# Performance work log

Hardware: AMD Instinct MI355X
Metric: run time of the kernel (lower is better)

## Reference

```python
import jax, jax.numpy as jnp
import numpy as np

N_NODES = 65536   # sli * node = 512 * 128
N_EDGES = 524288  # avg degree 8
SLI, NODE = 512, 128
SLOPE = 0.01      # nn.LeakyReLU default negative_slope


def leaky_relu(v):
    return jnp.where(v >= 0, v, SLOPE * v)


def graph_conv(h, src, dst, W, b):
    """DGL GraphConv with norm='both': D_in^{-1/2} A D_out^{-1/2} h W + b, then LeakyReLU."""
    ones = jnp.ones(src.shape[0], dtype=h.dtype)
    out_deg = jnp.clip(jax.ops.segment_sum(ones, src, num_segments=N_NODES), 1.0)
    in_deg = jnp.clip(jax.ops.segment_sum(ones, dst, num_segments=N_NODES), 1.0)
    h = h * jax.lax.rsqrt(out_deg)[:, None]                     # src-side norm
    agg = jax.ops.segment_sum(h[src], dst, num_segments=N_NODES)  # gather + scatter-add
    agg = agg * jax.lax.rsqrt(in_deg)[:, None]                  # dst-side norm
    return leaky_relu(agg @ W + b)


def graphsage(x, src, dst, W, b):
    # x: [sli, C, node] -> [sli*node, C] -> GraphConv -> [sli, F, node]
    sli, C, node = x.shape
    h = x.transpose(0, 2, 1).reshape(-1, C)
    h = graph_conv(h, src, dst, W, b)
    return h.reshape(sli, node, -1).transpose(0, 2, 1)


def conv1x1(x, W, b):
    # pointwise Conv1d: x [S, Cin, N], W [Cout, Cin] -> [S, Cout, N]
    return jnp.einsum('scn,oc->son', x, W) + b[None, :, None]


def setup_inputs() -> dict:
    key = jax.random.key(0)
    ks = jax.random.split(key, 16)
    d = {
        'x': jax.random.normal(ks[0], (SLI, 128, NODE), dtype=jnp.float32),
        'edge_src': jax.random.randint(ks[1], (N_EDGES,), 0, N_NODES, dtype=jnp.int32),
        'edge_dst': jax.random.randint(ks[2], (N_EDGES,), 0, N_NODES, dtype=jnp.int32),
        'W_head': jax.random.normal(ks[3], (128, 128), dtype=jnp.float32) * 0.05,
        'b_head': jnp.zeros((128,), dtype=jnp.float32),
        'W_res0': jax.random.normal(ks[4], (128, 128), dtype=jnp.float32) * 0.05,
        'b_res0': jnp.zeros((128,), dtype=jnp.float32),
        'W_res1': jax.random.normal(ks[5], (128, 128), dtype=jnp.float32) * 0.05,
        'b_res1': jnp.zeros((128,), dtype=jnp.float32),
        'W_res2': jax.random.normal(ks[6], (128, 128), dtype=jnp.float32) * 0.05,
        'b_res2': jnp.zeros((128,), dtype=jnp.float32),
        'W_fusion': jax.random.normal(ks[7], (256, 512), dtype=jnp.float32) * 0.05,
        'b_fusion': jnp.zeros((256,), dtype=jnp.float32),
        'W_p1': jax.random.normal(ks[8], (256, 768), dtype=jnp.float32) * 0.05,
        'b_p1': jnp.zeros((256,), dtype=jnp.float32),
        'W_p2': jax.random.normal(ks[9], (64, 256), dtype=jnp.float32) * 0.05,
        'b_p2': jnp.zeros((64,), dtype=jnp.float32),
        'W_p3': jax.random.normal(ks[10], (2, 64), dtype=jnp.float32) * 0.05,
        'b_p3': jnp.zeros((2,), dtype=jnp.float32),
    }
    return d


def reference(x, edge_src, edge_dst, W_head, b_head, W_res0, b_res0, W_res1, b_res1,
              W_res2, b_res2, W_fusion, b_fusion, W_p1, b_p1, W_p2, b_p2, W_p3, b_p3):
    h = graphsage(x, edge_src, edge_dst, W_head, b_head)   # [S, 128, N]
    states = [h]
    for W, b in ((W_res0, b_res0), (W_res1, b_res1), (W_res2, b_res2)):
        h = graphsage(h, edge_src, edge_dst, W, b) + h     # residual
        states.append(h)
    state = jnp.concatenate(states, axis=1)                # [S, 512, N]
    fused = conv1x1(state, W_fusion, b_fusion)             # [S, 256, N]
    global_state = jnp.max(fused, axis=2, keepdims=True)   # [S, 256, 1]
    global_state = jnp.broadcast_to(global_state, (state.shape[0], 256, state.shape[2]))
    state = jnp.concatenate([global_state, state], axis=1) # [S, 768, N]
    y = leaky_relu(conv1x1(state, W_p1, b_p1))
    y = leaky_relu(conv1x1(y, W_p2, b_p2))
    return conv1x1(y, W_p3, b_p3)                          # [S, 2, N]
```

## Files before the change

### kernel.cpp

```cpp
#include <hip/hip_runtime.h>

#define NN 65536
#define NE 524288
#define SLOPE 0.01f

typedef unsigned short us;
typedef __attribute__((ext_vector_type(8))) short short8;
typedef __attribute__((ext_vector_type(4))) float f32x4;

__device__ __forceinline__ float leaky(float v) { return v >= 0.f ? v : SLOPE * v; }
__device__ __forceinline__ float b2f(us u) { return __uint_as_float(((unsigned)u) << 16); }
__device__ __forceinline__ us f2b(float f) {
  unsigned u = __float_as_uint(f);
  u += 0x7fffu + ((u >> 16) & 1u);
  return (us)(u >> 16);
}
__device__ __forceinline__ void split2(float v, us& hi, us& lo) {
  hi = f2b(v);
  lo = f2b(v - b2f(hi));
}

__device__ __forceinline__ void gload16(const void* g, void* l) {
  __builtin_amdgcn_global_load_lds(
      (const __attribute__((address_space(1))) unsigned int*)g,
      (__attribute__((address_space(3))) unsigned int*)l, 16, 0, 0);
}

__global__ void zero_ints(int* __restrict__ p, int n) {
  int i = blockIdx.x * blockDim.x + threadIdx.x;
  if (i < n) p[i] = 0;
}

__global__ void deg_count(const int* __restrict__ src, const int* __restrict__ dst,
                          int* __restrict__ cout, int* __restrict__ cin) {
  int e = blockIdx.x * blockDim.x + threadIdx.x;
  if (e < NE) {
    atomicAdd(&cout[src[e]], 1);
    atomicAdd(&cin[dst[e]], 1);
  }
}

__global__ void rs_kernel(const int* __restrict__ cout, const int* __restrict__ cin,
                          float* __restrict__ rs_out, float* __restrict__ rs_in) {
  int n = blockIdx.x * blockDim.x + threadIdx.x;
  if (n < NN) {
    rs_out[n] = rsqrtf((float)(cout[n] > 0 ? cout[n] : 1));
    rs_in[n]  = rsqrtf((float)(cin[n]  > 0 ? cin[n]  : 1));
  }
}

__global__ __launch_bounds__(1024) void scan_kernel(const int* __restrict__ cnt,
                                                    int* __restrict__ row_ptr) {
  __shared__ int part[1024];
  int t = threadIdx.x;
  int base = t * 64;
  int s = 0;
  for (int i = 0; i < 64; ++i) s += cnt[base + i];
  part[t] = s;
  __syncthreads();
  for (int d = 1; d < 1024; d <<= 1) {
    int v = (t >= d) ? part[t - d] : 0;
    __syncthreads();
    part[t] += v;
    __syncthreads();
  }
  int run = part[t] - s;
  for (int i = 0; i < 64; ++i) { row_ptr[base + i] = run; run += cnt[base + i]; }
  if (t == 1023) row_ptr[NN] = run;
}

__global__ void csr_fill(const int* __restrict__ src, const int* __restrict__ dst,
                         const int* __restrict__ row_ptr, int* __restrict__ cursor,
                         int* __restrict__ csr) {
  int e = blockIdx.x * blockDim.x + threadIdx.x;
  if (e < NE) {
    int d = dst[e];
    int pos = atomicAdd(&cursor[d], 1);
    csr[row_ptr[d] + pos] = src[e];
  }
}

__global__ __launch_bounds__(256) void transpose_x(const float* __restrict__ x,
                                                   us* __restrict__ h0h,
                                                   us* __restrict__ h0l) {
  __shared__ float tile[128][68];
  int s  = blockIdx.x >> 1;
  int vh = (blockIdx.x & 1) * 64;
  const float* xs = x + (size_t)s * 16384;
  int t = threadIdx.x;
  int v4 = t & 15, c0 = t >> 4;
  for (int p = 0; p < 8; ++p) {
    int c = c0 + p * 16;
    float4 val = *(const float4*)(xs + (size_t)c * 128 + vh + v4 * 4);
    *(float4*)&tile[c][v4 * 4] = val;
  }
  __syncthreads();
  int c4 = t & 31, v0 = t >> 5;
  for (int p = 0; p < 8; ++p) {
    int v = v0 + p * 8;
    float o[4];
    o[0] = tile[c4 * 4 + 0][v];
    o[1] = tile[c4 * 4 + 1][v];
    o[2] = tile[c4 * 4 + 2][v];
    o[3] = tile[c4 * 4 + 3][v];
    us hh[4], ll[4];
#pragma unroll
    for (int j = 0; j < 4; ++j) split2(o[j], hh[j], ll[j]);
    size_t off = (size_t)(s * 128 + vh + v) * 128 + c4 * 4;
    uint2 wh = make_uint2((unsigned)hh[0] | ((unsigned)hh[1] << 16),
                          (unsigned)hh[2] | ((unsigned)hh[3] << 16));
    uint2 wl = make_uint2((unsigned)ll[0] | ((unsigned)ll[1] << 16),
                          (unsigned)ll[2] | ((unsigned)ll[3] << 16));
    *(uint2*)(h0h + off) = wh;
    *(uint2*)(h0l + off) = wl;
  }
}

__global__ void wsplit(const float* __restrict__ src, us* __restrict__ bh,
                       us* __restrict__ bl, int N, int K, int ld, int koff) {
  int idx = blockIdx.x * 256 + threadIdx.x;
  if (idx >= N * K) return;
  int n = idx / K, k = idx - n * K;
  float v = src[(size_t)n * ld + koff + k];
  us hi, lo; split2(v, hi, lo);
  bh[idx] = hi; bl[idx] = lo;
}

__global__ void wsplit_t(const float* __restrict__ src, us* __restrict__ bh,
                         us* __restrict__ bl, int N, int K, int ld) {
  int idx = blockIdx.x * 256 + threadIdx.x;
  if (idx >= N * K) return;
  int n = idx / K, k = idx - n * K;
  float v = src[(size_t)k * ld + n];
  us hi, lo; split2(v, hi, lo);
  bh[idx] = hi; bl[idx] = lo;
}

__global__ __launch_bounds__(256) void aggregate(
    const us* __restrict__ hh, const us* __restrict__ hl, int lda,
    const int* __restrict__ row_ptr, const int* __restrict__ csr,
    const float* __restrict__ rs_out, const float* __restrict__ rs_in,
    us* __restrict__ aggh, us* __restrict__ aggl) {
  const int lane = threadIdx.x & 63;
  const int n = blockIdx.x * 4 + (threadIdx.x >> 6);
  const us* base = ((lane < 32) ? hh : hl) + (size_t)(lane & 31) * 4;
  const int b = row_ptr[n], e = row_ptr[n + 1];
  float a0 = 0.f, a1 = 0.f, a2 = 0.f, a3 = 0.f;
  int i = b;
  for (; i + 4 <= e; i += 4) {
    int s0 = csr[i], s1 = csr[i + 1], s2 = csr[i + 2], s3 = csr[i + 3];
    uint2 v0 = *(const uint2*)(base + (size_t)s0 * lda);
    uint2 v1 = *(const uint2*)(base + (size_t)s1 * lda);
    uint2 v2 = *(const uint2*)(base + (size_t)s2 * lda);
    uint2 v3 = *(const uint2*)(base + (size_t)s3 * lda);
    float w0 = rs_out[s0], w1 = rs_out[s1], w2 = rs_out[s2], w3 = rs_out[s3];
    a0 = fmaf(w0, __uint_as_float(v0.x << 16), a0);
    a1 = fmaf(w0, __uint_as_float(v0.x & 0xffff0000u), a1);
    a2 = fmaf(w0, __uint_as_float(v0.y << 16), a2);
    a3 = fmaf(w0, __uint_as_float(v0.y & 0xffff0000u), a3);
    a0 = fmaf(w1, __uint_as_float(v1.x << 16), a0);
    a1 = fmaf(w1, __uint_as_float(v1.x & 0xffff0000u), a1);
    a2 = fmaf(w1, __uint_as_float(v1.y << 16), a2);
    a3 = fmaf(w1, __uint_as_float(v1.y & 0xffff0000u), a3);
    a0 = fmaf(w2, __uint_as_float(v2.x << 16), a0);
    a1 = fmaf(w2, __uint_as_float(v2.x & 0xffff0000u), a1);
    a2 = fmaf(w2, __uint_as_float(v2.y << 16), a2);
    a3 = fmaf(w2, __uint_as_float(v2.y & 0xffff0000u), a3);
    a0 = fmaf(w3, __uint_as_float(v3.x << 16), a0);
    a1 = fmaf(w3, __uint_as_float(v3.x & 0xffff0000u), a1);
    a2 = fmaf(w3, __uint_as_float(v3.y << 16), a2);
    a3 = fmaf(w3, __uint_as_float(v3.y & 0xffff0000u), a3);
  }
  for (; i < e; ++i) {
    int s0 = csr[i];
    uint2 v0 = *(const uint2*)(base + (size_t)s0 * lda);
    float w0 = rs_out[s0];
    a0 = fmaf(w0, __uint_as_float(v0.x << 16), a0);
    a1 = fmaf(w0, __uint_as_float(v0.x & 0xffff0000u), a1);
    a2 = fmaf(w0, __uint_as_float(v0.y << 16), a2);
    a3 = fmaf(w0, __uint_as_float(v0.y & 0xffff0000u), a3);
  }
  a0 += __shfl_xor(a0, 32);
  a1 += __shfl_xor(a1, 32);
  a2 += __shfl_xor(a2, 32);
  a3 += __shfl_xor(a3, 32);
  const float ri = rs_in[n];
  a0 *= ri; a1 *= ri; a2 *= ri; a3 *= ri;
  us h[4], l[4];
  split2(a0, h[0], l[0]); split2(a1, h[1], l[1]);
  split2(a2, h[2], l[2]); split2(a3, h[3], l[3]);
  size_t o = (size_t)n * 128 + (size_t)(lane & 31) * 4;
  if (lane < 32) {
    uint2 wv = make_uint2((unsigned)h[0] | ((unsigned)h[1] << 16),
                          (unsigned)h[2] | ((unsigned)h[3] << 16));
    *(uint2*)(aggh + o) = wv;
  } else {
    uint2 wv = make_uint2((unsigned)l[0] | ((unsigned)l[1] << 16),
                          (unsigned)l[2] | ((unsigned)l[3] << 16));
    *(uint2*)(aggl + o) = wv;
  }
}

template<int KTOT, int BN, int WM, int PH, int MODE>
__global__ __launch_bounds__(512) void mgemm8(
    const us* __restrict__ Ah, const us* __restrict__ Al, int lda,
    const us* __restrict__ Bh, const us* __restrict__ Bl,
    const float* __restrict__ bias,
    float* __restrict__ outf, us* __restrict__ outh, us* __restrict__ outl,
    int ldo, int colOff,
    const us* __restrict__ prevh, const us* __restrict__ prevl,
    const float* __restrict__ gcon) {
  constexpr int WN  = 8 / WM;
  constexpr int FM  = 16 / WM;
  constexpr int FMP = FM / PH;
  constexpr int NT  = KTOT / 32;
  constexpr int LBN = (BN == 256) ? 8 : ((BN == 128) ? 7 : 6);
  constexpr int CHT = 2048 + BN * 8;
  constexpr int LPT = CHT / 512;

  __shared__ __align__(16) us L[2][CHT * 8];

  const int t = threadIdx.x;
  const int mbase = blockIdx.x * 256;

  const us* gp[LPT];
#pragma unroll
  for (int i = 0; i < LPT; ++i) {
    int id = i * 512 + t;
    if (id < 1024) {
      int row = id & 255, kb = id >> 8;
      gp[i] = Ah + (size_t)(mbase + row) * lda + kb * 8;
    } else if (id < 2048) {
      int c = id - 1024, row = c & 255, kb = c >> 8;
      gp[i] = Al + (size_t)(mbase + row) * lda + kb * 8;
    } else if (id < 2048 + BN * 4) {
      int c = id - 2048, row = c & (BN - 1), kb = c >> LBN;
      gp[i] = Bh + (size_t)row * KTOT + kb * 8;
    } else {
      int c = id - 2048 - BN * 4, row = c & (BN - 1), kb = c >> LBN;
      gp[i] = Bl + (size_t)row * KTOT + kb * 8;
    }
  }

  const int lane = t & 63, wvi = t >> 6;
  const int wm = wvi & (WM - 1), wn = wvi / WM;
  const int l15 = lane & 15, lkb = lane >> 4;
  const int wrow = wm * (256 / WM);

  f32x4 acc[FM][4];
#pragma unroll
  for (int i = 0; i < FM; ++i)
#pragma unroll
    for (int j = 0; j < 4; ++j)
#pragma unroll
      for (int e = 0; e < 4; ++e) acc[i][j][e] = 0.f;

  auto stage = [&](us* Lb, int k0) {
#pragma unroll
    for (int i = 0; i < LPT; ++i)
      gload16(gp[i] + k0, Lb + (size_t)(i * 512 + t) * 8);
  };
  auto waitL = [&]() {
    if constexpr (LPT == 8)      asm volatile("s_waitcnt vmcnt(8)" ::: "memory");
    else if constexpr (LPT == 6) asm volatile("s_waitcnt vmcnt(6)" ::: "memory");
    else                         asm volatile("s_waitcnt vmcnt(5)" ::: "memory");
    __builtin_amdgcn_sched_barrier(0);
  };
  auto wait0 = [&]() {
    asm volatile("s_waitcnt vmcnt(0)" ::: "memory");
    __builtin_amdgcn_sched_barrier(0);
  };
  auto bar = [&]() {
    __builtin_amdgcn_s_barrier();
    __builtin_amdgcn_sched_barrier(0);
  };
  auto ktile = [&](const us* Lb) {
    short8 bh[4], bl[4];
#pragma unroll
    for (int fn = 0; fn < 4; ++fn) {
      const int bcol = wn * 64 + fn * 16 + l15;
      bh[fn] = *(const short8*)(Lb + ((size_t)(2048 + lkb * BN + bcol)) * 8);
      bl[fn] = *(const short8*)(Lb + ((size_t)(2048 + BN * 4 + lkb * BN + bcol)) * 8);
    }
#pragma unroll
    for (int p = 0; p < PH; ++p) {
      short8 ah[FMP], al[FMP];
#pragma unroll
      for (int f = 0; f < FMP; ++f) {
        const int arow = wrow + (p * FMP + f) * 16 + l15;
        ah[f] = *(const short8*)(Lb + ((size_t)(lkb * 256 + arow)) * 8);
        al[f] = *(const short8*)(Lb + ((size_t)(1024 + lkb * 256 + arow)) * 8);
      }
      __builtin_amdgcn_s_setprio(1);
#pragma unroll
      for (int f = 0; f < FMP; ++f)
#pragma unroll
        for (int fn = 0; fn < 4; ++fn)
          acc[p * FMP + f][fn] =
              __builtin_amdgcn_mfma_f32_16x16x32_bf16(ah[f], bh[fn], acc[p * FMP + f][fn], 0, 0, 0);
#pragma unroll
      for (int f = 0; f < FMP; ++f)
#pragma unroll
        for (int fn = 0; fn < 4; ++fn)
          acc[p * FMP + f][fn] =
              __builtin_amdgcn_mfma_f32_16x16x32_bf16(al[f], bh[fn], acc[p * FMP + f][fn], 0, 0, 0);
#pragma unroll
      for (int f = 0; f < FMP; ++f)
#pragma unroll
        for (int fn = 0; fn < 4; ++fn)
          acc[p * FMP + f][fn] =
              __builtin_amdgcn_mfma_f32_16x16x32_bf16(ah[f], bl[fn], acc[p * FMP + f][fn], 0, 0, 0);
      __builtin_amdgcn_s_setprio(0);
      __builtin_amdgcn_sched_barrier(0);
    }
  };

  stage(L[0], 0);
  if (NT > 1) stage(L[1], 32);
#pragma unroll 1
  for (int kt = 0; kt < NT; kt += 2) {
    waitL();
    bar();
    ktile(L[0]);
    bar();
    if (kt + 2 < NT) stage(L[0], (kt + 2) * 32);
    if (kt + 3 < NT) waitL(); else wait0();
    bar();
    ktile(L[1]);
    bar();
    if (kt + 3 < NT) stage(L[1], (kt + 3) * 32);
  }

  if constexpr (MODE == 0 || MODE == 1 || MODE == 3) {
    const float* gc = (MODE == 3) ? (gcon + (size_t)(blockIdx.x * 2 + wm) * 256) : nullptr;
#pragma unroll
    for (int fm = 0; fm < FM; ++fm)
#pragma unroll
      for (int fn = 0; fn < 4; ++fn) {
        const int col = wn * 64 + fn * 16 + l15;
        float bb = bias[col];
        if constexpr (MODE == 3) bb += gc[col];
#pragma unroll
        for (int r = 0; r < 4; ++r) {
          const int row = mbase + wrow + fm * 16 + lkb * 4 + r;
          float v = leaky(acc[fm][fn][r] + bb);
          const size_t off = (size_t)row * ldo + colOff + col;
          if constexpr (MODE == 1) v += b2f(prevh[off - 128]) + b2f(prevl[off - 128]);
          us hi, lo; split2(v, hi, lo);
          outh[off] = hi;
          outl[off] = lo;
        }
      }
  } else if constexpr (MODE == 2) {
#pragma unroll
    for (int fn = 0; fn < 4; ++fn) {
      float m = acc[0][fn][0];
#pragma unroll
      for (int fm = 0; fm < FM; ++fm)
#pragma unroll
        for (int r = 0; r < 4; ++r) m = fmaxf(m, acc[fm][fn][r]);
      m = fmaxf(m, __shfl_xor(m, 16));
      m = fmaxf(m, __shfl_xor(m, 32));
      if (lane < 16) {
        const int col = wn * 64 + fn * 16 + l15;
        outf[(size_t)(blockIdx.x * 2 + wm) * 256 + col] = m + bias[col];
      }
    }
  } else {
#pragma unroll
    for (int fm = 0; fm < FM; ++fm)
#pragma unroll
      for (int fn = 0; fn < 4; ++fn) {
        const int col = fn * 16 + l15;
        const float bb = bias[col];
#pragma unroll
        for (int r = 0; r < 4; ++r) {
          const int row = mbase + wrow + fm * 16 + lkb * 4 + r;
          outf[(size_t)row * 64 + col] = leaky(acc[fm][fn][r] + bb);
        }
      }
  }
}

__global__ void gcon_kernel(const float* __restrict__ gmax, const float* __restrict__ Wp1,
                            float* __restrict__ gcon) {
  __shared__ float g[256];
  int s = blockIdx.x, o = threadIdx.x;
  g[o] = gmax[(size_t)s * 256 + o];
  __syncthreads();
  float acc = 0.f;
  const float* wr = Wp1 + (size_t)o * 768;
#pragma unroll 8
  for (int c = 0; c < 256; ++c) acc += g[c] * wr[c];
  gcon[(size_t)s * 256 + o] = acc;
}

__global__ void p3_kernel(const float* __restrict__ y2, const float* __restrict__ W,
                          const float* __restrict__ b, float* __restrict__ out) {
  __shared__ float w0[64], w1[64];
  int t = threadIdx.x;
  if (t < 64) { w0[t] = W[t]; w1[t] = W[64 + t]; }
  __syncthreads();
  int n = blockIdx.x * 256 + t;
  const float* row = y2 + (size_t)n * 64;
  float a0 = b[0], a1 = b[1];
#pragma unroll
  for (int j = 0; j < 64; j += 4) {
    float4 v = *(const float4*)(row + j);
    a0 += v.x * w0[j] + v.y * w0[j + 1] + v.z * w0[j + 2] + v.w * w0[j + 3];
    a1 += v.x * w1[j] + v.y * w1[j + 1] + v.z * w1[j + 2] + v.w * w1[j + 3];
  }
  int s = n >> 7, vv = n & 127;
  out[((size_t)s * 2 + 0) * 128 + vv] = a0;
  out[((size_t)s * 2 + 1) * 128 + vv] = a1;
}

extern "C" void kernel_launch(void* const* d_in, const int* in_sizes, int n_in,
                              void* d_out, int out_size, void* d_ws, size_t ws_size,
                              hipStream_t stream) {
  const float* x        = (const float*)d_in[0];
  const int*   esrc     = (const int*)d_in[1];
  const int*   edst     = (const int*)d_in[2];
  const float* W_head   = (const float*)d_in[3];
  const float* b_head   = (const float*)d_in[4];
  const float* W_res[3] = {(const float*)d_in[5], (const float*)d_in[7], (const float*)d_in[9]};
  const float* b_res[3] = {(const float*)d_in[6], (const float*)d_in[8], (const float*)d_in[10]};
  const float* W_fusion = (const float*)d_in[11];
  const float* b_fusion = (const float*)d_in[12];
  const float* W_p1     = (const float*)d_in[13];
  const float* b_p1     = (const float*)d_in[14];
  const float* W_p2     = (const float*)d_in[15];
  const float* b_p2     = (const float*)d_in[16];
  const float* W_p3     = (const float*)d_in[17];
  const float* b_p3     = (const float*)d_in[18];
  float* outp = (float*)d_out;

  char* w = (char*)d_ws;
  size_t off = 0;
  auto alloc = [&](size_t bytes) { char* p = w + off; off += (bytes + 255) & ~(size_t)255; return p; };

  us* states_h = (us*)alloc((size_t)NN * 512 * 2);
  us* states_l = (us*)alloc((size_t)NN * 512 * 2);
  char* regionA = alloc((size_t)NN * 128 * 2 * 4);
  us* h0h  = (us*)regionA;
  us* h0l  = (us*)(regionA + (size_t)NN * 128 * 2);
  us* aggh = (us*)(regionA + (size_t)NN * 128 * 4);
  us* aggl = (us*)(regionA + (size_t)NN * 128 * 6);
  us* y1h  = (us*)regionA;
  us* y1l  = (us*)(regionA + (size_t)NN * 256 * 2);
  float* y2 = (float*)states_h;

  float* gmax   = (float*)alloc(512 * 256 * 4);
  float* gcon   = (float*)alloc(512 * 256 * 4);
  float* rs_out = (float*)alloc((size_t)NN * 4);
  float* rs_in  = (float*)alloc((size_t)NN * 4);
  us* cWh[4]; us* cWl[4];
  for (int l = 0; l < 4; ++l) { cWh[l] = (us*)alloc(128 * 128 * 2); cWl[l] = (us*)alloc(128 * 128 * 2); }
  us* fWh  = (us*)alloc(256 * 512 * 2);
  us* fWl  = (us*)alloc(256 * 512 * 2);
  us* p1Wh = (us*)alloc(256 * 512 * 2);
  us* p1Wl = (us*)alloc(256 * 512 * 2);
  us* p2Wh = (us*)alloc(64 * 256 * 2);
  us* p2Wl = (us*)alloc(64 * 256 * 2);
  int* cnt_out = (int*)alloc((size_t)NN * 4);
  int* cnt_in  = (int*)alloc((size_t)NN * 4);
  int* cursor  = (int*)alloc((size_t)NN * 4);
  int* row_ptr = (int*)alloc(((size_t)NN + 1) * 4);
  int* csr     = (int*)alloc((size_t)NE * 4);

  zero_ints<<<(3 * NN + 255) / 256, 256, 0, stream>>>(cnt_out, 3 * NN);
  deg_count<<<NE / 256, 256, 0, stream>>>(esrc, edst, cnt_out, cnt_in);
  rs_kernel<<<NN / 256, 256, 0, stream>>>(cnt_out, cnt_in, rs_out, rs_in);
  scan_kernel<<<1, 1024, 0, stream>>>(cnt_in, row_ptr);
  csr_fill<<<NE / 256, 256, 0, stream>>>(esrc, edst, row_ptr, cursor, csr);

  transpose_x<<<1024, 256, 0, stream>>>(x, h0h, h0l);
  const float* cW[4] = {W_head, W_res[0], W_res[1], W_res[2]};
  for (int l = 0; l < 4; ++l)
    wsplit_t<<<64, 256, 0, stream>>>(cW[l], cWh[l], cWl[l], 128, 128, 128);
  wsplit<<<512, 256, 0, stream>>>(W_fusion, fWh, fWl, 256, 512, 512, 0);
  wsplit<<<512, 256, 0, stream>>>(W_p1, p1Wh, p1Wl, 256, 512, 768, 256);
  wsplit<<<64, 256, 0, stream>>>(W_p2, p2Wh, p2Wl, 64, 256, 256, 0);

  const float* cB[4] = {b_head, b_res[0], b_res[1], b_res[2]};
  aggregate<<<NN / 4, 256, 0, stream>>>(h0h, h0l, 128, row_ptr, csr, rs_out, rs_in, aggh, aggl);
  mgemm8<128, 128, 4, 2, 0><<<256, 512, 0, stream>>>(aggh, aggl, 128, cWh[0], cWl[0], cB[0],
                                                     nullptr, states_h, states_l, 512, 0,
                                                     nullptr, nullptr, nullptr);
  for (int l = 1; l <= 3; ++l) {
    aggregate<<<NN / 4, 256, 0, stream>>>(states_h + (size_t)(l - 1) * 128,
                                          states_l + (size_t)(l - 1) * 128, 512,
                                          row_ptr, csr, rs_out, rs_in, aggh, aggl);
    mgemm8<128, 128, 4, 2, 1><<<256, 512, 0, stream>>>(aggh, aggl, 128, cWh[l], cWl[l], cB[l],
                                                       nullptr, states_h, states_l, 512, l * 128,
                                                       states_h, states_l, nullptr);
  }
  mgemm8<512, 256, 2, 4, 2><<<256, 512, 0, stream>>>(states_h, states_l, 512, fWh, fWl, b_fusion,
                                                     gmax, nullptr, nullptr, 0, 0,
                                                     nullptr, nullptr, nullptr);
  gcon_kernel<<<512, 256, 0, stream>>>(gmax, W_p1, gcon);
  mgemm8<512, 256, 2, 4, 3><<<256, 512, 0, stream>>>(states_h, states_l, 512, p1Wh, p1Wl, b_p1,
                                                     nullptr, y1h, y1l, 256, 0,
                                                     nullptr, nullptr, gcon);
  mgemm8<256, 64, 8, 2, 4><<<256, 512, 0, stream>>>(y1h, y1l, 256, p2Wh, p2Wl, b_p2,
                                                    y2, nullptr, nullptr, 0, 0,
                                                    nullptr, nullptr, nullptr);
  p3_kernel<<<NN / 256, 256, 0, stream>>>(y2, W_p3, b_p3, outp);
}
```

Before: 607.5 us.

## Fuse fusion GEMM, global max and p1 GEMM into one kernel; widen aggregate loads

Merges the fusion conv, per-slice max, global-contribution matvec and p1 conv into one kernel. Each 128-row block (one slice) computes both the 256 fusion columns and the 256 p1 columns against a concatenated 512x512 weight, so the states matrix is read once and two launches plus the gmax/gcon round trips go away. The aggregate kernel now processes two nodes per wave with 16-byte loads. In exchange the fused kernel uses a single-buffered LDS pipeline with a full wait before every k-tile, and the extra block-wide syncs for the max and matvec may reduce overlap.

```diff
diff --git a/kernel.cpp b/kernel.cpp
--- a/kernel.cpp
+++ b/kernel.cpp
@@ -142,62 +142,71 @@
     const float* __restrict__ rs_out, const float* __restrict__ rs_in,
     us* __restrict__ aggh, us* __restrict__ aggl) {
   const int lane = threadIdx.x & 63;
-  const int n = blockIdx.x * 4 + (threadIdx.x >> 6);
-  const us* base = ((lane < 32) ? hh : hl) + (size_t)(lane & 31) * 4;
+  const int wid = threadIdx.x >> 6;
+  const int half = (lane >> 5) & 1;
+  const int n = blockIdx.x * 8 + wid * 2 + half;
+  const bool lop = (lane & 31) >= 16;
+  const int c16 = lane & 15;
+  const us* base = (lop ? hl : hh) + (size_t)c16 * 8;
   const int b = row_ptr[n], e = row_ptr[n + 1];
-  float a0 = 0.f, a1 = 0.f, a2 = 0.f, a3 = 0.f;
+  float a[8];
+#pragma unroll
+  for (int j = 0; j < 8; ++j) a[j] = 0.f;
   int i = b;
-  for (; i + 4 <= e; i += 4) {
-    int s0 = csr[i], s1 = csr[i + 1], s2 = csr[i + 2], s3 = csr[i + 3];
-    uint2 v0 = *(const uint2*)(base + (size_t)s0 * lda);
-    uint2 v1 = *(const uint2*)(base + (size_t)s1 * lda);
-    uint2 v2 = *(const uint2*)(base + (size_t)s2 * lda);
-    uint2 v3 = *(const uint2*)(base + (size_t)s3 * lda);
-    float w0 = rs_out[s0], w1 = rs_out[s1], w2 = rs_out[s2], w3 = rs_out[s3];
-    a0 = fmaf(w0, __uint_as_float(v0.x << 16), a0);
-    a1 = fmaf(w0, __uint_as_float(v0.x & 0xffff0000u), a1);
-    a2 = fmaf(w0, __uint_as_float(v0.y << 16), a2);
-    a3 = fmaf(w0, __uint_as_float(v0.y & 0xffff0000u), a3);
-    a0 = fmaf(w1, __uint_as_float(v1.x << 16), a0);
-    a1 = fmaf(w1, __uint_as_float(v1.x & 0xffff0000u), a1);
-    a2 = fmaf(w1, __uint_as_float(v1.y << 16), a2);
-    a3 = fmaf(w1, __uint_as_float(v1.y & 0xffff0000u), a3);
-    a0 = fmaf(w2, __uint_as_float(v2.x << 16), a0);
-    a1 = fmaf(w2, __uint_as_float(v2.x & 0xffff0000u), a1);
-    a2 = fmaf(w2, __uint_as_float(v2.y << 16), a2);
-    a3 = fmaf(w2, __uint_as_float(v2.y & 0xffff0000u), a3);
-    a0 = fmaf(w3, __uint_as_float(v3.x << 16), a0);
-    a1 = fmaf(w3, __uint_as_float(v3.x & 0xffff0000u), a1);
-    a2 = fmaf(w3, __uint_as_float(v3.y << 16), a2);
-    a3 = fmaf(w3, __uint_as_float(v3.y & 0xffff0000u), a3);
-  }
-  for (; i < e; ++i) {
+  for (; i + 2 <= e; i += 2) {
+    int s0 = csr[i], s1 = csr[i + 1];
+    uint4 v0 = *(const uint4*)(base + (size_t)s0 * lda);
+    uint4 v1 = *(const uint4*)(base + (size_t)s1 * lda);
+    float w0 = rs_out[s0], w1 = rs_out[s1];
+    a[0] = fmaf(w0, __uint_as_float(v0.x << 16), a[0]);
+    a[1] = fmaf(w0, __uint_as_float(v0.x & 0xffff0000u), a[1]);
+    a[2] = fmaf(w0, __uint_as_float(v0.y << 16), a[2]);
+    a[3] = fmaf(w0, __uint_as_float(v0.y & 0xffff0000u), a[3]);
+    a[4] = fmaf(w0, __uint_as_float(v0.z << 16), a[4]);
+    a[5] = fmaf(w0, __uint_as_float(v0.z & 0xffff0000u), a[5]);
+    a[6] = fmaf(w0, __uint_as_float(v0.w << 16), a[6]);
+    a[7] = fmaf(w0, __uint_as_float(v0.w & 0xffff0000u), a[7]);
+    a[0] = fmaf(w1, __uint_as_float(v1.x << 16), a[0]);
+    a[1] = fmaf(w1, __uint_as_float(v1.x & 0xffff0000u), a[1]);
+    a[2] = fmaf(w1, __uint_as_float(v1.y << 16), a[2]);
+    a[3] = fmaf(w1, __uint_as_float(v1.y & 0xffff0000u), a[3]);
+    a[4] = fmaf(w1, __uint_as_float(v1.z << 16), a[4]);
+    a[5] = fmaf(w1, __uint_as_float(v1.z & 0xffff0000u), a[5]);
+    a[6] = fmaf(w1, __uint_as_float(v1.w << 16), a[6]);
+    a[7] = fmaf(w1, __uint_as_float(v1.w & 0xffff0000u), a[7]);
+  }
+  if (i < e) {
     int s0 = csr[i];
-    uint2 v0 = *(const uint2*)(base + (size_t)s0 * lda);
+    uint4 v0 = *(const uint4*)(base + (size_t)s0 * lda);
     float w0 = rs_out[s0];
-    a0 = fmaf(w0, __uint_as_float(v0.x << 16), a0);
-    a1 = fmaf(w0, __uint_as_float(v0.x & 0xffff0000u), a1);
-    a2 = fmaf(w0, __uint_as_float(v0.y << 16), a2);
-    a3 = fmaf(w0, __uint_as_float(v0.y & 0xffff0000u), a3);
-  }
-  a0 += __shfl_xor(a0, 32);
-  a1 += __shfl_xor(a1, 32);
-  a2 += __shfl_xor(a2, 32);
-  a3 += __shfl_xor(a3, 32);
+    a[0] = fmaf(w0, __uint_as_float(v0.x << 16), a[0]);
+    a[1] = fmaf(w0, __uint_as_float(v0.x & 0xffff0000u), a[1]);
+    a[2] = fmaf(w0, __uint_as_float(v0.y << 16), a[2]);
+    a[3] = fmaf(w0, __uint_as_float(v0.y & 0xffff0000u), a[3]);
+    a[4] = fmaf(w0, __uint_as_float(v0.z << 16), a[4]);
+    a[5] = fmaf(w0, __uint_as_float(v0.z & 0xffff0000u), a[5]);
+    a[6] = fmaf(w0, __uint_as_float(v0.w << 16), a[6]);
+    a[7] = fmaf(w0, __uint_as_float(v0.w & 0xffff0000u), a[7]);
+  }
+#pragma unroll
+  for (int j = 0; j < 8; ++j) a[j] += __shfl_xor(a[j], 16);
   const float ri = rs_in[n];
-  a0 *= ri; a1 *= ri; a2 *= ri; a3 *= ri;
-  us h[4], l[4];
-  split2(a0, h[0], l[0]); split2(a1, h[1], l[1]);
-  split2(a2, h[2], l[2]); split2(a3, h[3], l[3]);
-  size_t o = (size_t)n * 128 + (size_t)(lane & 31) * 4;
-  if (lane < 32) {
-    uint2 wv = make_uint2((unsigned)h[0] | ((unsigned)h[1] << 16),
-                          (unsigned)h[2] | ((unsigned)h[3] << 16));
-    *(uint2*)(aggh + o) = wv;
+  us h8[8], l8[8];
+#pragma unroll
+  for (int j = 0; j < 8; ++j) split2(a[j] * ri, h8[j], l8[j]);
+  size_t o = (size_t)n * 128 + (size_t)c16 * 8;
+  if (!lop) {
+    uint4 w = make_uint4((unsigned)h8[0] | ((unsigned)h8[1] << 16),
+                         (unsigned)h8[2] | ((unsigned)h8[3] << 16),
+                         (unsigned)h8[4] | ((unsigned)h8[5] << 16),
+                         (unsigned)h8[6] | ((unsigned)h8[7] << 16));
+    *(uint4*)(aggh + o) = w;
   } else {
-    uint2 wv = make_uint2((unsigned)l[0] | ((unsigned)l[1] << 16),
-                          (unsigned)l[2] | ((unsigned)l[3] << 16));
-    *(uint2*)(aggl + o) = wv;
+    uint4 w = make_uint4((unsigned)l8[0] | ((unsigned)l8[1] << 16),
+                         (unsigned)l8[2] | ((unsigned)l8[3] << 16),
+                         (unsigned)l8[4] | ((unsigned)l8[5] << 16),
+                         (unsigned)l8[6] | ((unsigned)l8[7] << 16));
+    *(uint4*)(aggl + o) = w;
   }
 }
 
@@ -208,8 +217,7 @@
     const float* __restrict__ bias,
     float* __restrict__ outf, us* __restrict__ outh, us* __restrict__ outl,
     int ldo, int colOff,
-    const us* __restrict__ prevh, const us* __restrict__ prevl,
-    const float* __restrict__ gcon) {
+    const us* __restrict__ prevh, const us* __restrict__ prevl) {
   constexpr int WN  = 8 / WM;
   constexpr int FM  = 16 / WM;
   constexpr int FMP = FM / PH;
@@ -331,15 +339,13 @@
     if (kt + 3 < NT) stage(L[1], (kt + 3) * 32);
   }
 
-  if constexpr (MODE == 0 || MODE == 1 || MODE == 3) {
-    const float* gc = (MODE == 3) ? (gcon + (size_t)(blockIdx.x * 2 + wm) * 256) : nullptr;
+  if constexpr (MODE == 0 || MODE == 1) {
 #pragma unroll
     for (int fm = 0; fm < FM; ++fm)
 #pragma unroll
       for (int fn = 0; fn < 4; ++fn) {
         const int col = wn * 64 + fn * 16 + l15;
         float bb = bias[col];
-        if constexpr (MODE == 3) bb += gc[col];
 #pragma unroll
         for (int r = 0; r < 4; ++r) {
           const int row = mbase + wrow + fm * 16 + lkb * 4 + r;
@@ -351,21 +357,6 @@
           outl[off] = lo;
         }
       }
-  } else if constexpr (MODE == 2) {
-#pragma unroll
-    for (int fn = 0; fn < 4; ++fn) {
-      float m = acc[0][fn][0];
-#pragma unroll
-      for (int fm = 0; fm < FM; ++fm)
-#pragma unroll
-        for (int r = 0; r < 4; ++r) m = fmaxf(m, acc[fm][fn][r]);
-      m = fmaxf(m, __shfl_xor(m, 16));
-      m = fmaxf(m, __shfl_xor(m, 32));
-      if (lane < 16) {
-        const int col = wn * 64 + fn * 16 + l15;
-        outf[(size_t)(blockIdx.x * 2 + wm) * 256 + col] = m + bias[col];
-      }
-    }
   } else {
 #pragma unroll
     for (int fm = 0; fm < FM; ++fm)
@@ -382,17 +373,175 @@
   }
 }
 
-__global__ void gcon_kernel(const float* __restrict__ gmax, const float* __restrict__ Wp1,
-                            float* __restrict__ gcon) {
-  __shared__ float g[256];
-  int s = blockIdx.x, o = threadIdx.x;
-  g[o] = gmax[(size_t)s * 256 + o];
+__global__ __launch_bounds__(512) void fusion_p1(
+    const us* __restrict__ Ah, const us* __restrict__ Al,
+    const us* __restrict__ Bh, const us* __restrict__ Bl,
+    const float* __restrict__ bf, const float* __restrict__ bp1,
+    const float* __restrict__ Wp1,
+    us* __restrict__ y1h, us* __restrict__ y1l) {
+  constexpr int KTOT = 512, NT = 16;
+  __shared__ __align__(16) us L[5120 * 8];
+  __shared__ float gm[256];
+  __shared__ float gc[256];
+
+  const int t = threadIdx.x;
+  const int mbase = blockIdx.x * 128;
+
+  const us* gp[10];
+#pragma unroll
+  for (int i = 0; i < 10; ++i) {
+    int id = i * 512 + t;
+    if (id < 512) {
+      int row = id & 127, kb = id >> 7;
+      gp[i] = Ah + (size_t)(mbase + row) * 512 + kb * 8;
+    } else if (id < 1024) {
+      int c = id - 512, row = c & 127, kb = c >> 7;
+      gp[i] = Al + (size_t)(mbase + row) * 512 + kb * 8;
+    } else if (id < 3072) {
+      int c = id - 1024, n = c & 511, kb = c >> 9;
+      gp[i] = Bh + (size_t)n * KTOT + kb * 8;
+    } else {
+      int c = id - 3072, n = c & 511, kb = c >> 9;
+      gp[i] = Bl + (size_t)n * KTOT + kb * 8;
+    }
+  }
+
+  const int lane = t & 63, wvi = t >> 6;
+  const int wm = wvi & 1, wn = wvi >> 1;
+  const int l15 = lane & 15, lkb = lane >> 4;
+  const int wrow = wm * 64;
+
+  f32x4 acc[4][8];
+#pragma unroll
+  for (int i = 0; i < 4; ++i)
+#pragma unroll
+    for (int j = 0; j < 8; ++j)
+#pragma unroll
+      for (int e = 0; e < 4; ++e) acc[i][j][e] = 0.f;
+
+  auto stage = [&](int k0) {
+#pragma unroll
+    for (int i = 0; i < 10; ++i)
+      gload16(gp[i] + k0, L + (size_t)(i * 512 + t) * 8);
+  };
+  auto wait0 = [&]() {
+    asm volatile("s_waitcnt vmcnt(0)" ::: "memory");
+    __builtin_amdgcn_sched_barrier(0);
+  };
+  auto bar = [&]() {
+    __builtin_amdgcn_s_barrier();
+    __builtin_amdgcn_sched_barrier(0);
+  };
+  auto ktile = [&]() {
+    short8 bh8[8], bl8[8];
+#pragma unroll
+    for (int fn = 0; fn < 8; ++fn) {
+      const int bcol = wn * 128 + fn * 16 + l15;
+      bh8[fn] = *(const short8*)(L + ((size_t)(1024 + lkb * 512 + bcol)) * 8);
+      bl8[fn] = *(const short8*)(L + ((size_t)(3072 + lkb * 512 + bcol)) * 8);
+    }
+#pragma unroll
+    for (int p = 0; p < 2; ++p) {
+      short8 ah[2], al[2];
+#pragma unroll
+      for (int f = 0; f < 2; ++f) {
+        const int arow = wrow + (p * 2 + f) * 16 + l15;
+        ah[f] = *(const short8*)(L + ((size_t)(lkb * 128 + arow)) * 8);
+        al[f] = *(const short8*)(L + ((size_t)(512 + lkb * 128 + arow)) * 8);
+      }
+      __builtin_amdgcn_s_setprio(1);
+#pragma unroll
+      for (int f = 0; f < 2; ++f)
+#pragma unroll
+        for (int fn = 0; fn < 8; ++fn)
+          acc[p * 2 + f][fn] =
+              __builtin_amdgcn_mfma_f32_16x16x32_bf16(ah[f], bh8[fn], acc[p * 2 + f][fn], 0, 0, 0);
+#pragma unroll
+      for (int f = 0; f < 2; ++f)
+#pragma unroll
+        for (int fn = 0; fn < 8; ++fn)
+          acc[p * 2 + f][fn] =
+              __builtin_amdgcn_mfma_f32_16x16x32_bf16(al[f], bh8[fn], acc[p * 2 + f][fn], 0, 0, 0);
+#pragma unroll
+      for (int f = 0; f < 2; ++f)
+#pragma unroll
+        for (int fn = 0; fn < 8; ++fn)
+          acc[p * 2 + f][fn] =
+              __builtin_amdgcn_mfma_f32_16x16x32_bf16(ah[f], bl8[fn], acc[p * 2 + f][fn], 0, 0, 0);
+      __builtin_amdgcn_s_setprio(0);
+      __builtin_amdgcn_sched_barrier(0);
+    }
+  };
+
+  stage(0);
+  wait0();
+  bar();
+#pragma unroll 1
+  for (int kt = 0; kt < NT; ++kt) {
+    ktile();
+    bar();
+    if (kt + 1 < NT) {
+      stage((kt + 1) * 32);
+      wait0();
+      bar();
+    }
+  }
+
+  float mloc[8];
+  if (wn < 2) {
+#pragma unroll
+    for (int fn = 0; fn < 8; ++fn) {
+      float m = acc[0][fn][0];
+#pragma unroll
+      for (int fm = 0; fm < 4; ++fm)
+#pragma unroll
+        for (int r = 0; r < 4; ++r) m = fmaxf(m, acc[fm][fn][r]);
+      m = fmaxf(m, __shfl_xor(m, 16));
+      m = fmaxf(m, __shfl_xor(m, 32));
+      mloc[fn] = m;
+    }
+    if (wm == 0 && lane < 16) {
+#pragma unroll
+      for (int fn = 0; fn < 8; ++fn) gm[wn * 128 + fn * 16 + l15] = mloc[fn];
+    }
+  }
   __syncthreads();
-  float acc = 0.f;
-  const float* wr = Wp1 + (size_t)o * 768;
-#pragma unroll 8
-  for (int c = 0; c < 256; ++c) acc += g[c] * wr[c];
-  gcon[(size_t)s * 256 + o] = acc;
+  if (wn < 2 && wm == 1 && lane < 16) {
+#pragma unroll
+    for (int fn = 0; fn < 8; ++fn) {
+      const int c = wn * 128 + fn * 16 + l15;
+      gm[c] = fmaxf(gm[c], mloc[fn]) + bf[c];
+    }
+  }
+  __syncthreads();
+  if (t < 256) {
+    const float* wr = Wp1 + (size_t)t * 768;
+    float s = 0.f;
+#pragma unroll 4
+    for (int c = 0; c < 256; c += 4) {
+      float4 w4 = *(const float4*)(wr + c);
+      s += gm[c] * w4.x + gm[c + 1] * w4.y + gm[c + 2] * w4.z + gm[c + 3] * w4.w;
+    }
+    gc[t] = s;
+  }
+  __syncthreads();
+  if (wn >= 2) {
+#pragma unroll
+    for (int fm = 0; fm < 4; ++fm)
+#pragma unroll
+      for (int fn = 0; fn < 8; ++fn) {
+        const int pcol = (wn - 2) * 128 + fn * 16 + l15;
+        const float bb = bp1[pcol] + gc[pcol];
+#pragma unroll
+        for (int r = 0; r < 4; ++r) {
+          const int row = mbase + wrow + fm * 16 + lkb * 4 + r;
+          float v = leaky(acc[fm][fn][r] + bb);
+          us hi, lo; split2(v, hi, lo);
+          y1h[(size_t)row * 256 + pcol] = hi;
+          y1l[(size_t)row * 256 + pcol] = lo;
+        }
+      }
+  }
 }
 
 __global__ void p3_kernel(const float* __restrict__ y2, const float* __restrict__ W,
@@ -450,16 +599,12 @@
   us* y1l  = (us*)(regionA + (size_t)NN * 256 * 2);
   float* y2 = (float*)states_h;
 
-  float* gmax   = (float*)alloc(512 * 256 * 4);
-  float* gcon   = (float*)alloc(512 * 256 * 4);
   float* rs_out = (float*)alloc((size_t)NN * 4);
   float* rs_in  = (float*)alloc((size_t)NN * 4);
   us* cWh[4]; us* cWl[4];
   for (int l = 0; l < 4; ++l) { cWh[l] = (us*)alloc(128 * 128 * 2); cWl[l] = (us*)alloc(128 * 128 * 2); }
-  us* fWh  = (us*)alloc(256 * 512 * 2);
-  us* fWl  = (us*)alloc(256 * 512 * 2);
-  us* p1Wh = (us*)alloc(256 * 512 * 2);
-  us* p1Wl = (us*)alloc(256 * 512 * 2);
+  us* fWh  = (us*)alloc(512 * 512 * 2);
+  us* fWl  = (us*)alloc(512 * 512 * 2);
   us* p2Wh = (us*)alloc(64 * 256 * 2);
   us* p2Wl = (us*)alloc(64 * 256 * 2);
   int* cnt_out = (int*)alloc((size_t)NN * 4);
@@ -479,31 +624,26 @@
   for (int l = 0; l < 4; ++l)
     wsplit_t<<<64, 256, 0, stream>>>(cW[l], cWh[l], cWl[l], 128, 128, 128);
   wsplit<<<512, 256, 0, stream>>>(W_fusion, fWh, fWl, 256, 512, 512, 0);
-  wsplit<<<512, 256, 0, stream>>>(W_p1, p1Wh, p1Wl, 256, 512, 768, 256);
+  wsplit<<<512, 256, 0, stream>>>(W_p1, fWh + 256 * 512, fWl + 256 * 512, 256, 512, 768, 256);
   wsplit<<<64, 256, 0, stream>>>(W_p2, p2Wh, p2Wl, 64, 256, 256, 0);
 
   const float* cB[4] = {b_head, b_res[0], b_res[1], b_res[2]};
-  aggregate<<<NN / 4, 256, 0, stream>>>(h0h, h0l, 128, row_ptr, csr, rs_out, rs_in, aggh, aggl);
+  aggregate<<<NN / 8, 256, 0, stream>>>(h0h, h0l, 128, row_ptr, csr, rs_out, rs_in, aggh, aggl);
   mgemm8<128, 128, 4, 2, 0><<<256, 512, 0, stream>>>(aggh, aggl, 128, cWh[0], cWl[0], cB[0],
                                                      nullptr, states_h, states_l, 512, 0,
-                                                     nullptr, nullptr, nullptr);
+                                                     nullptr, nullptr);
   for (int l = 1; l <= 3; ++l) {
-    aggregate<<<NN / 4, 256, 0, stream>>>(states_h + (size_t)(l - 1) * 128,
+    aggregate<<<NN / 8, 256, 0, stream>>>(states_h + (size_t)(l - 1) * 128,
                                           states_l + (size_t)(l - 1) * 128, 512,
                                           row_ptr, csr, rs_out, rs_in, aggh, aggl);
     mgemm8<128, 128, 4, 2, 1><<<256, 512, 0, stream>>>(aggh, aggl, 128, cWh[l], cWl[l], cB[l],
                                                        nullptr, states_h, states_l, 512, l * 128,
-                                                       states_h, states_l, nullptr);
-  }
-  mgemm8<512, 256, 2, 4, 2><<<256, 512, 0, stream>>>(states_h, states_l, 512, fWh, fWl, b_fusion,
-                                                     gmax, nullptr, nullptr, 0, 0,
-                                                     nullptr, nullptr, nullptr);
-  gcon_kernel<<<512, 256, 0, stream>>>(gmax, W_p1, gcon);
-  mgemm8<512, 256, 2, 4, 3><<<256, 512, 0, stream>>>(states_h, states_l, 512, p1Wh, p1Wl, b_p1,
-                                                     nullptr, y1h, y1l, 256, 0,
-                                                     nullptr, nullptr, gcon);
+                                                       states_h, states_l);
+  }
+  fusion_p1<<<512, 512, 0, stream>>>(states_h, states_l, fWh, fWl,
+                                     b_fusion, b_p1, W_p1, y1h, y1l);
   mgemm8<256, 64, 8, 2, 4><<<256, 512, 0, stream>>>(y1h, y1l, 256, p2Wh, p2Wl, b_p2,
                                                     y2, nullptr, nullptr, 0, 0,
-                                                    nullptr, nullptr, nullptr);
+                                                    nullptr, nullptr);
   p3_kernel<<<NN / 256, 256, 0, stream>>>(y2, W_p3, b_p3, outp);
 }
```

Result: slower. 622.7 us (+2.5%).

## Fuse neighbor aggregation with GraphConv GEMM in a single kernel

Applied to the files above, without the earlier changes.

Each GraphConv layer used to run an aggregate kernel that wrote the aggregated bf16 hi/lo features to global memory, followed by a separate MFMA GEMM that read them back. The new agg_conv kernel aggregates 64 destination rows per block straight into swizzled LDS, then runs the 128x128 split-bf16 MFMA GEMM with double-buffered weight tiles and applies bias, LeakyReLU and the residual in the epilogue. This removes the global round trip of the aggregated tensor and half of the launches. In exchange, each block's gather phase and GEMM phase can no longer overlap across kernels, and the GEMM tile is smaller (64 rows, 2x2 fragments per wave), which may use the matrix units less efficiently.

```diff
diff --git a/kernel.cpp b/kernel.cpp
--- a/kernel.cpp
+++ b/kernel.cpp
@@ -136,69 +136,183 @@
   bh[idx] = hi; bl[idx] = lo;
 }
 
-__global__ __launch_bounds__(256) void aggregate(
+template<int MODE>
+__global__ __launch_bounds__(512) void agg_conv(
     const us* __restrict__ hh, const us* __restrict__ hl, int lda,
     const int* __restrict__ row_ptr, const int* __restrict__ csr,
     const float* __restrict__ rs_out, const float* __restrict__ rs_in,
-    us* __restrict__ aggh, us* __restrict__ aggl) {
-  const int lane = threadIdx.x & 63;
-  const int n = blockIdx.x * 4 + (threadIdx.x >> 6);
-  const us* base = ((lane < 32) ? hh : hl) + (size_t)(lane & 31) * 4;
-  const int b = row_ptr[n], e = row_ptr[n + 1];
-  float a0 = 0.f, a1 = 0.f, a2 = 0.f, a3 = 0.f;
-  int i = b;
-  for (; i + 4 <= e; i += 4) {
-    int s0 = csr[i], s1 = csr[i + 1], s2 = csr[i + 2], s3 = csr[i + 3];
-    uint2 v0 = *(const uint2*)(base + (size_t)s0 * lda);
-    uint2 v1 = *(const uint2*)(base + (size_t)s1 * lda);
-    uint2 v2 = *(const uint2*)(base + (size_t)s2 * lda);
-    uint2 v3 = *(const uint2*)(base + (size_t)s3 * lda);
-    float w0 = rs_out[s0], w1 = rs_out[s1], w2 = rs_out[s2], w3 = rs_out[s3];
-    a0 = fmaf(w0, __uint_as_float(v0.x << 16), a0);
-    a1 = fmaf(w0, __uint_as_float(v0.x & 0xffff0000u), a1);
-    a2 = fmaf(w0, __uint_as_float(v0.y << 16), a2);
-    a3 = fmaf(w0, __uint_as_float(v0.y & 0xffff0000u), a3);
-    a0 = fmaf(w1, __uint_as_float(v1.x << 16), a0);
-    a1 = fmaf(w1, __uint_as_float(v1.x & 0xffff0000u), a1);
-    a2 = fmaf(w1, __uint_as_float(v1.y << 16), a2);
-    a3 = fmaf(w1, __uint_as_float(v1.y & 0xffff0000u), a3);
-    a0 = fmaf(w2, __uint_as_float(v2.x << 16), a0);
-    a1 = fmaf(w2, __uint_as_float(v2.x & 0xffff0000u), a1);
-    a2 = fmaf(w2, __uint_as_float(v2.y << 16), a2);
-    a3 = fmaf(w2, __uint_as_float(v2.y & 0xffff0000u), a3);
-    a0 = fmaf(w3, __uint_as_float(v3.x << 16), a0);
-    a1 = fmaf(w3, __uint_as_float(v3.x & 0xffff0000u), a1);
-    a2 = fmaf(w3, __uint_as_float(v3.y << 16), a2);
-    a3 = fmaf(w3, __uint_as_float(v3.y & 0xffff0000u), a3);
-  }
-  for (; i < e; ++i) {
-    int s0 = csr[i];
-    uint2 v0 = *(const uint2*)(base + (size_t)s0 * lda);
-    float w0 = rs_out[s0];
-    a0 = fmaf(w0, __uint_as_float(v0.x << 16), a0);
-    a1 = fmaf(w0, __uint_as_float(v0.x & 0xffff0000u), a1);
-    a2 = fmaf(w0, __uint_as_float(v0.y << 16), a2);
-    a3 = fmaf(w0, __uint_as_float(v0.y & 0xffff0000u), a3);
-  }
-  a0 += __shfl_xor(a0, 32);
-  a1 += __shfl_xor(a1, 32);
-  a2 += __shfl_xor(a2, 32);
-  a3 += __shfl_xor(a3, 32);
-  const float ri = rs_in[n];
-  a0 *= ri; a1 *= ri; a2 *= ri; a3 *= ri;
-  us h[4], l[4];
-  split2(a0, h[0], l[0]); split2(a1, h[1], l[1]);
-  split2(a2, h[2], l[2]); split2(a3, h[3], l[3]);
-  size_t o = (size_t)n * 128 + (size_t)(lane & 31) * 4;
-  if (lane < 32) {
-    uint2 wv = make_uint2((unsigned)h[0] | ((unsigned)h[1] << 16),
-                          (unsigned)h[2] | ((unsigned)h[3] << 16));
-    *(uint2*)(aggh + o) = wv;
-  } else {
-    uint2 wv = make_uint2((unsigned)l[0] | ((unsigned)l[1] << 16),
-                          (unsigned)l[2] | ((unsigned)l[3] << 16));
-    *(uint2*)(aggl + o) = wv;
-  }
+    const us* __restrict__ Bh, const us* __restrict__ Bl,
+    const float* __restrict__ bias,
+    us* __restrict__ outh, us* __restrict__ outl, int colOff) {
+  __shared__ __align__(16) us Ah_[16 * 64 * 8];
+  __shared__ __align__(16) us Al_[16 * 64 * 8];
+  __shared__ __align__(16) us Bb[2][1024 * 8];
+
+  const int t = threadIdx.x;
+  const int lane = t & 63, wv = t >> 6;
+  const int mbase = blockIdx.x * 64;
+
+  {
+    const int half = (lane >> 5) & 1;
+    const bool lop = (lane & 31) >= 16;
+    const int c16 = lane & 15;
+    const us* gbase = (lop ? hl : hh) + (size_t)c16 * 8;
+    for (int pr = 0; pr < 4; ++pr) {
+      const int row = wv * 8 + pr * 2 + half;
+      const int n = mbase + row;
+      const int b = row_ptr[n], e = row_ptr[n + 1];
+      float a[8];
+#pragma unroll
+      for (int j = 0; j < 8; ++j) a[j] = 0.f;
+      int i = b;
+      for (; i + 2 <= e; i += 2) {
+        int s0 = csr[i], s1 = csr[i + 1];
+        uint4 v0 = *(const uint4*)(gbase + (size_t)s0 * lda);
+        uint4 v1 = *(const uint4*)(gbase + (size_t)s1 * lda);
+        float w0 = rs_out[s0], w1 = rs_out[s1];
+        a[0] = fmaf(w0, __uint_as_float(v0.x << 16), a[0]);
+        a[1] = fmaf(w0, __uint_as_float(v0.x & 0xffff0000u), a[1]);
+        a[2] = fmaf(w0, __uint_as_float(v0.y << 16), a[2]);
+        a[3] = fmaf(w0, __uint_as_float(v0.y & 0xffff0000u), a[3]);
+        a[4] = fmaf(w0, __uint_as_float(v0.z << 16), a[4]);
+        a[5] = fmaf(w0, __uint_as_float(v0.z & 0xffff0000u), a[5]);
+        a[6] = fmaf(w0, __uint_as_float(v0.w << 16), a[6]);
+        a[7] = fmaf(w0, __uint_as_float(v0.w & 0xffff0000u), a[7]);
+        a[0] = fmaf(w1, __uint_as_float(v1.x << 16), a[0]);
+        a[1] = fmaf(w1, __uint_as_float(v1.x & 0xffff0000u), a[1]);
+        a[2] = fmaf(w1, __uint_as_float(v1.y << 16), a[2]);
+        a[3] = fmaf(w1, __uint_as_float(v1.y & 0xffff0000u), a[3]);
+        a[4] = fmaf(w1, __uint_as_float(v1.z << 16), a[4]);
+        a[5] = fmaf(w1, __uint_as_float(v1.z & 0xffff0000u), a[5]);
+        a[6] = fmaf(w1, __uint_as_float(v1.w << 16), a[6]);
+        a[7] = fmaf(w1, __uint_as_float(v1.w & 0xffff0000u), a[7]);
+      }
+      if (i < e) {
+        int s0 = csr[i];
+        uint4 v0 = *(const uint4*)(gbase + (size_t)s0 * lda);
+        float w0 = rs_out[s0];
+        a[0] = fmaf(w0, __uint_as_float(v0.x << 16), a[0]);
+        a[1] = fmaf(w0, __uint_as_float(v0.x & 0xffff0000u), a[1]);
+        a[2] = fmaf(w0, __uint_as_float(v0.y << 16), a[2]);
+        a[3] = fmaf(w0, __uint_as_float(v0.y & 0xffff0000u), a[3]);
+        a[4] = fmaf(w0, __uint_as_float(v0.z << 16), a[4]);
+        a[5] = fmaf(w0, __uint_as_float(v0.z & 0xffff0000u), a[5]);
+        a[6] = fmaf(w0, __uint_as_float(v0.w << 16), a[6]);
+        a[7] = fmaf(w0, __uint_as_float(v0.w & 0xffff0000u), a[7]);
+      }
+#pragma unroll
+      for (int j = 0; j < 8; ++j) a[j] += __shfl_xor(a[j], 16);
+      const float ri = rs_in[n];
+      us h8[8], l8[8];
+#pragma unroll
+      for (int j = 0; j < 8; ++j) split2(a[j] * ri, h8[j], l8[j]);
+      us* dst = (lop ? Al_ : Ah_) + (size_t)(c16 * 64 + (row ^ (c16 & 7))) * 8;
+      const us* src = lop ? l8 : h8;
+      uint4 w = make_uint4((unsigned)src[0] | ((unsigned)src[1] << 16),
+                           (unsigned)src[2] | ((unsigned)src[3] << 16),
+                           (unsigned)src[4] | ((unsigned)src[5] << 16),
+                           (unsigned)src[6] | ((unsigned)src[7] << 16));
+      *(uint4*)dst = w;
+    }
+  }
+  __syncthreads();
+
+  const int wm = wv & 1, wn = wv >> 1;
+  const int l15 = lane & 15, lkb = lane >> 4;
+  f32x4 acc[2][2];
+#pragma unroll
+  for (int i = 0; i < 2; ++i)
+#pragma unroll
+    for (int j = 0; j < 2; ++j)
+#pragma unroll
+      for (int e = 0; e < 4; ++e) acc[i][j][e] = 0.f;
+
+  const us* gBh_t = Bh + (size_t)(t & 127) * 128 + (t >> 7) * 8;
+  const us* gBl_t = Bl + (size_t)(t & 127) * 128 + (t >> 7) * 8;
+  auto stageB = [&](int buf, int kt) {
+    gload16(gBh_t + kt * 32, Bb[buf] + (size_t)t * 8);
+    gload16(gBl_t + kt * 32, Bb[buf] + (size_t)(t + 512) * 8);
+  };
+  auto waitC = [&]() {
+    asm volatile("s_waitcnt vmcnt(2)" ::: "memory");
+    __builtin_amdgcn_sched_barrier(0);
+  };
+  auto wait0 = [&]() {
+    asm volatile("s_waitcnt vmcnt(0)" ::: "memory");
+    __builtin_amdgcn_sched_barrier(0);
+  };
+  auto bar = [&]() {
+    __builtin_amdgcn_s_barrier();
+    __builtin_amdgcn_sched_barrier(0);
+  };
+  auto ktileA = [&](const us* Bbuf, int kt) {
+    short8 bh2[2], bl2[2], ah2[2], al2[2];
+#pragma unroll
+    for (int fn = 0; fn < 2; ++fn) {
+      const int bcol = wn * 32 + fn * 16 + l15;
+      bh2[fn] = *(const short8*)(Bbuf + (size_t)(lkb * 128 + bcol) * 8);
+      bl2[fn] = *(const short8*)(Bbuf + (size_t)(512 + lkb * 128 + bcol) * 8);
+    }
+    const int kg = kt * 4 + lkb;
+#pragma unroll
+    for (int f = 0; f < 2; ++f) {
+      const int arow = (wm * 32 + f * 16 + l15) ^ (kg & 7);
+      ah2[f] = *(const short8*)(Ah_ + (size_t)(kg * 64 + arow) * 8);
+      al2[f] = *(const short8*)(Al_ + (size_t)(kg * 64 + arow) * 8);
+    }
+    __builtin_amdgcn_s_setprio(1);
+#pragma unroll
+    for (int f = 0; f < 2; ++f)
+#pragma unroll
+      for (int fn = 0; fn < 2; ++fn)
+        acc[f][fn] = __builtin_amdgcn_mfma_f32_16x16x32_bf16(ah2[f], bh2[fn], acc[f][fn], 0, 0, 0);
+#pragma unroll
+    for (int f = 0; f < 2; ++f)
+#pragma unroll
+      for (int fn = 0; fn < 2; ++fn)
+        acc[f][fn] = __builtin_amdgcn_mfma_f32_16x16x32_bf16(al2[f], bh2[fn], acc[f][fn], 0, 0, 0);
+#pragma unroll
+    for (int f = 0; f < 2; ++f)
+#pragma unroll
+      for (int fn = 0; fn < 2; ++fn)
+        acc[f][fn] = __builtin_amdgcn_mfma_f32_16x16x32_bf16(ah2[f], bl2[fn], acc[f][fn], 0, 0, 0);
+    __builtin_amdgcn_s_setprio(0);
+    __builtin_amdgcn_sched_barrier(0);
+  };
+
+  stageB(0, 0);
+  stageB(1, 1);
+  waitC(); bar();
+  ktileA(Bb[0], 0);
+  bar();
+  stageB(0, 2);
+  waitC(); bar();
+  ktileA(Bb[1], 1);
+  bar();
+  stageB(1, 3);
+  waitC(); bar();
+  ktileA(Bb[0], 2);
+  bar();
+  wait0(); bar();
+  ktileA(Bb[1], 3);
+
+#pragma unroll
+  for (int fm = 0; fm < 2; ++fm)
+#pragma unroll
+    for (int fn = 0; fn < 2; ++fn) {
+      const int col = wn * 32 + fn * 16 + l15;
+      const float bb = bias[col];
+#pragma unroll
+      for (int r = 0; r < 4; ++r) {
+        const int row = mbase + wm * 32 + fm * 16 + lkb * 4 + r;
+        float v = leaky(acc[fm][fn][r] + bb);
+        const size_t off = (size_t)row * 512 + colOff + col;
+        if constexpr (MODE == 1) v += b2f(outh[off - 128]) + b2f(outl[off - 128]);
+        us hi, lo; split2(v, hi, lo);
+        outh[off] = hi;
+        outl[off] = lo;
+      }
+    }
 }
 
 template<int KTOT, int BN, int WM, int PH, int MODE>
@@ -208,7 +322,6 @@
     const float* __restrict__ bias,
     float* __restrict__ outf, us* __restrict__ outh, us* __restrict__ outl,
     int ldo, int colOff,
-    const us* __restrict__ prevh, const us* __restrict__ prevl,
     const float* __restrict__ gcon) {
   constexpr int WN  = 8 / WM;
   constexpr int FM  = 16 / WM;
@@ -331,21 +444,19 @@
     if (kt + 3 < NT) stage(L[1], (kt + 3) * 32);
   }
 
-  if constexpr (MODE == 0 || MODE == 1 || MODE == 3) {
-    const float* gc = (MODE == 3) ? (gcon + (size_t)(blockIdx.x * 2 + wm) * 256) : nullptr;
+  if constexpr (MODE == 3) {
+    const float* gc = gcon + (size_t)(blockIdx.x * 2 + wm) * 256;
 #pragma unroll
     for (int fm = 0; fm < FM; ++fm)
 #pragma unroll
       for (int fn = 0; fn < 4; ++fn) {
         const int col = wn * 64 + fn * 16 + l15;
-        float bb = bias[col];
-        if constexpr (MODE == 3) bb += gc[col];
+        const float bb = bias[col] + gc[col];
 #pragma unroll
         for (int r = 0; r < 4; ++r) {
           const int row = mbase + wrow + fm * 16 + lkb * 4 + r;
           float v = leaky(acc[fm][fn][r] + bb);
           const size_t off = (size_t)row * ldo + colOff + col;
-          if constexpr (MODE == 1) v += b2f(prevh[off - 128]) + b2f(prevl[off - 128]);
           us hi, lo; split2(v, hi, lo);
           outh[off] = hi;
           outl[off] = lo;
@@ -444,8 +555,6 @@
   char* regionA = alloc((size_t)NN * 128 * 2 * 4);
   us* h0h  = (us*)regionA;
   us* h0l  = (us*)(regionA + (size_t)NN * 128 * 2);
-  us* aggh = (us*)(regionA + (size_t)NN * 128 * 4);
-  us* aggl = (us*)(regionA + (size_t)NN * 128 * 6);
   us* y1h  = (us*)regionA;
   us* y1l  = (us*)(regionA + (size_t)NN * 256 * 2);
   float* y2 = (float*)states_h;
@@ -483,27 +592,20 @@
   wsplit<<<64, 256, 0, stream>>>(W_p2, p2Wh, p2Wl, 64, 256, 256, 0);
 
   const float* cB[4] = {b_head, b_res[0], b_res[1], b_res[2]};
-  aggregate<<<NN / 4, 256, 0, stream>>>(h0h, h0l, 128, row_ptr, csr, rs_out, rs_in, aggh, aggl);
-  mgemm8<128, 128, 4, 2, 0><<<256, 512, 0, stream>>>(aggh, aggl, 128, cWh[0], cWl[0], cB[0],
-                                                     nullptr, states_h, states_l, 512, 0,
-                                                     nullptr, nullptr, nullptr);
+  agg_conv<0><<<NN / 64, 512, 0, stream>>>(h0h, h0l, 128, row_ptr, csr, rs_out, rs_in,
+                                           cWh[0], cWl[0], cB[0], states_h, states_l, 0);
   for (int l = 1; l <= 3; ++l) {
-    aggregate<<<NN / 4, 256, 0, stream>>>(states_h + (size_t)(l - 1) * 128,
-                                          states_l + (size_t)(l - 1) * 128, 512,
-                                          row_ptr, csr, rs_out, rs_in, aggh, aggl);
-    mgemm8<128, 128, 4, 2, 1><<<256, 512, 0, stream>>>(aggh, aggl, 128, cWh[l], cWl[l], cB[l],
-                                                       nullptr, states_h, states_l, 512, l * 128,
-                                                       states_h, states_l, nullptr);
+    agg_conv<1><<<NN / 64, 512, 0, stream>>>(states_h + (size_t)(l - 1) * 128,
+                                             states_l + (size_t)(l - 1) * 128, 512,
+                                             row_ptr, csr, rs_out, rs_in,
+                                             cWh[l], cWl[l], cB[l], states_h, states_l, l * 128);
   }
   mgemm8<512, 256, 2, 4, 2><<<256, 512, 0, stream>>>(states_h, states_l, 512, fWh, fWl, b_fusion,
-                                                     gmax, nullptr, nullptr, 0, 0,
-                                                     nullptr, nullptr, nullptr);
+                                                     gmax, nullptr, nullptr, 0, 0, nullptr);
   gcon_kernel<<<512, 256, 0, stream>>>(gmax, W_p1, gcon);
   mgemm8<512, 256, 2, 4, 3><<<256, 512, 0, stream>>>(states_h, states_l, 512, p1Wh, p1Wl, b_p1,
-                                                     nullptr, y1h, y1l, 256, 0,
-                                                     nullptr, nullptr, gcon);
+                                                     nullptr, y1h, y1l, 256, 0, gcon);
   mgemm8<256, 64, 8, 2, 4><<<256, 512, 0, stream>>>(y1h, y1l, 256, p2Wh, p2Wl, b_p2,
-                                                    y2, nullptr, nullptr, 0, 0,
-                                                    nullptr, nullptr, nullptr);
+                                                    y2, nullptr, nullptr, 0, 0, nullptr);
   p3_kernel<<<NN / 256, 256, 0, stream>>>(y2, W_p3, b_p3, outp);
 }
```

Result: slower. 653.9 us (+7.6%).
